# Kernel tuning notes

Hardware: AMD Instinct MI355X
Metric: run time of the kernel (lower is better)

Reference implementation:

```python
import jax, jax.numpy as jnp
import numpy as np

N_NODES = 100000
N_EDGES = 1600000
N_GRAPHS = 256
EPS = 1e-5  # GraphNorm / BatchNorm eps


def _seg_sum(x, seg, n):
    return jax.ops.segment_sum(x, seg, num_segments=n)


def setup_inputs() -> dict:
    key = jax.random.key(0)
    ks = jax.random.split(key, 24)
    f32 = jnp.float32

    def nrm(k, shape, s=0.05):
        return jax.random.normal(k, shape, f32) * s

    inp = {}
    inp["x"] = jax.random.normal(ks[0], (N_NODES, 64), f32)
    inp["edge_attr"] = jax.random.normal(ks[1], (N_EDGES, 8), f32)
    # edge_mlp: Linear(8,16) -> ReLU -> Linear(16,1); final bias +2 keeps degrees positive
    inp["em_w1"] = nrm(ks[2], (16, 8), 0.1); inp["em_b1"] = jnp.zeros((16,), f32)
    inp["em_w2"] = nrm(ks[3], (1, 16), 0.1); inp["em_b2"] = jnp.full((1,), 2.0, f32)
    # GCNConv weights stored (in, out); PyG GCNConv lin has no bias, separate bias after aggregation
    inp["conv_w0"] = nrm(ks[4], (64, 128)); inp["conv_b0"] = jnp.zeros((128,), f32)
    inp["conv_w1"] = nrm(ks[5], (128, 128)); inp["conv_b1"] = jnp.zeros((128,), f32)
    inp["conv_w2"] = nrm(ks[6], (128, 128)); inp["conv_b2"] = jnp.zeros((128,), f32)
    # GraphNorm params: weight=1, bias=0, mean_scale=1 (PyG init)
    for i in range(3):
        inp[f"gn_w{i}"] = jnp.ones((128,), f32)
        inp[f"gn_b{i}"] = jnp.zeros((128,), f32)
        inp[f"gn_ms{i}"] = jnp.ones((128,), f32)
    # MLP head (weights stored (in,out)); BatchNorm1d eval: running_mean=0, running_var=1
    inp["lin_w0"] = nrm(ks[7], (128, 256)); inp["lin_b0"] = jnp.zeros((256,), f32)
    inp["bn_g0"] = jnp.ones((256,), f32); inp["bn_b0"] = jnp.zeros((256,), f32)
    inp["lin_w1"] = nrm(ks[8], (256, 128)); inp["lin_b1"] = jnp.zeros((128,), f32)
    inp["bn_g1"] = jnp.ones((128,), f32); inp["bn_b1"] = jnp.zeros((128,), f32)
    inp["out_w"] = nrm(ks[9], (128, 1)); inp["out_b"] = jnp.zeros((1,), f32)
    inp["edge_index"] = jax.random.randint(ks[10], (2, N_EDGES), 0, N_NODES)
    inp["batch"] = jnp.sort(jax.random.randint(ks[11], (N_NODES,), 0, N_GRAPHS))
    return inp


def _gcn_conv(h, W, b, src, tgt, ew):
    # PyG GCNConv with edge_weight: add self-loops (weight 1), symmetric normalization
    hw = h @ W  # [N, out]
    deg = _seg_sum(ew, tgt, N_NODES) + 1.0  # in-degree incl. self-loop
    dinv = jnp.where(deg > 0, jax.lax.rsqrt(deg), 0.0)
    norm_e = dinv[src] * ew * dinv[tgt]  # [E]
    agg = _seg_sum(norm_e[:, None] * hw[src], tgt, N_NODES)
    agg = agg + (dinv * dinv)[:, None] * hw  # self-loop contribution
    return agg + b


def _graph_norm(h, batch, w, b, ms, cnt):
    mean = _seg_sum(h, batch, N_GRAPHS) / cnt[:, None]  # [G, C]
    sub = h - ms * mean[batch]
    var = _seg_sum(sub * sub, batch, N_GRAPHS) / cnt[:, None]
    return w * sub / jnp.sqrt(var + EPS)[batch] + b


def reference(x, edge_attr, em_w1, em_b1, em_w2, em_b2,
              conv_w0, conv_b0, conv_w1, conv_b1, conv_w2, conv_b2,
              gn_w0, gn_b0, gn_ms0, gn_w1, gn_b1, gn_ms1, gn_w2, gn_b2, gn_ms2,
              lin_w0, lin_b0, bn_g0, bn_b0, lin_w1, lin_b1, bn_g1, bn_b1,
              out_w, out_b, edge_index, batch):
    src, tgt = edge_index[0], edge_index[1]
    ew = (jax.nn.relu(edge_attr @ em_w1.T + em_b1) @ em_w2.T + em_b2).reshape(-1)  # [E]
    cnt = jnp.maximum(_seg_sum(jnp.ones((N_NODES,), x.dtype), batch, N_GRAPHS), 1.0)

    h = x
    layers = [(conv_w0, conv_b0, gn_w0, gn_b0, gn_ms0),
              (conv_w1, conv_b1, gn_w1, gn_b1, gn_ms1),
              (conv_w2, conv_b2, gn_w2, gn_b2, gn_ms2)]
    for W, b, gw, gb, gms in layers:
        h = _gcn_conv(h, W, b, src, tgt, ew)
        h = _graph_norm(h, batch, gw, gb, gms, cnt)
        h = jax.nn.relu(h)  # dropout is identity in eval mode

    pooled = _seg_sum(h, batch, N_GRAPHS) / cnt[:, None]  # global_mean_pool [G, 128]

    inv = 1.0 / jnp.sqrt(1.0 + EPS)  # BatchNorm1d eval: mean=0, var=1
    h = jax.nn.relu((pooled @ lin_w0 + lin_b0) * inv * bn_g0 + bn_b0)
    h = jax.nn.relu((h @ lin_w1 + lin_b1) * inv * bn_g1 + bn_b1)
    out = h @ out_w + out_b  # [G, 1]
    return (out, h)
```

## Files before the change

kernel.cpp:

```cpp
#include <hip/hip_runtime.h>

#define N_NODES 100000
#define N_EDGES 1600000
#define N_GRAPHS 256
#define EPS 1e-5f

#define SCAN_BLOCKS ((N_NODES + 255) / 256)

#define EB 6250
#define WB 128
#define W0B 32
#define PREP_BLOCKS (EB + WB + W0B + 2)

typedef __attribute__((ext_vector_type(8))) short bfrag8;
typedef __attribute__((ext_vector_type(4))) float facc4;

__device__ __forceinline__ void fma4(float4& a, float s, const float4& w) {
  a.x += s * w.x; a.y += s * w.y; a.z += s * w.z; a.w += s * w.w;
}

__device__ __forceinline__ unsigned short f2bf(float f) {
  union { float f; unsigned u; } x;
  x.f = f;
  unsigned r = x.u + 0x7FFF + ((x.u >> 16) & 1);
  return (unsigned short)(r >> 16);
}
__device__ __forceinline__ unsigned packbf(float a, float b) {
  return (unsigned)f2bf(a) | ((unsigned)f2bf(b) << 16);
}
__device__ __forceinline__ float4 bf4(unsigned lo, unsigned hi) {
  union { unsigned u; float f; } a, b, c, d;
  a.u = lo << 16;
  b.u = lo & 0xFFFF0000u;
  c.u = hi << 16;
  d.u = hi & 0xFFFF0000u;
  return make_float4(a.f, b.f, c.f, d.f);
}
__device__ __forceinline__ float bfat(const unsigned* tb, int idx) {
  unsigned u = tb[idx >> 1];
  union { unsigned u; float f; } v;
  v.u = (idx & 1) ? (u & 0xFFFF0000u) : (u << 16);
  return v.f;
}

__global__ __launch_bounds__(256) void k_prep(
    const float* __restrict__ ea, const float* __restrict__ w1,
    const float* __restrict__ b1, const float* __restrict__ w2,
    const float* __restrict__ b2, const int* __restrict__ tgt,
    float* __restrict__ ew, int* __restrict__ rowcnt, int* __restrict__ rank,
    const float* __restrict__ cw1, const float* __restrict__ cw2,
    unsigned short* __restrict__ wt1, unsigned short* __restrict__ wt2,
    const float* __restrict__ cw0, unsigned short* __restrict__ wt0,
    const int* __restrict__ batch, int* __restrict__ start) {
  __shared__ float W1[128], B1[16], W2[16];
  const int b = blockIdx.x;
  const int t = threadIdx.x;
  if (b < EB) {
    if (t < 128) W1[t] = w1[t];
    if (t < 16) { B1[t] = b1[t]; W2[t] = w2[t]; }
    __syncthreads();
    int e = b * 256 + t;
    if (e >= N_EDGES) return;
    const float4* ap = (const float4*)(ea + (size_t)e * 8);
    float4 a0 = ap[0], a1 = ap[1];
    float a[8] = {a0.x, a0.y, a0.z, a0.w, a1.x, a1.y, a1.z, a1.w};
    float out = b2[0];
#pragma unroll
    for (int i = 0; i < 16; ++i) {
      float h = B1[i];
#pragma unroll
      for (int j = 0; j < 8; ++j) h += a[j] * W1[i * 8 + j];
      out += fmaxf(h, 0.f) * W2[i];
    }
    ew[e] = out;
    rank[e] = atomicAdd(&rowcnt[tgt[e]], 1);
  } else if (b < EB + WB) {
    int lb = b - EB;
    int half = lb >> 6;
    int id = (lb & 63) * 256 + t;
    const float* w = half ? cw2 : cw1;
    unsigned short* o = half ? wt2 : wt1;
    int n = id >> 7, k = id & 127;
    o[n * 128 + k] = f2bf(w[k * 128 + n]);
  } else if (b < EB + WB + W0B) {
    int id = (b - EB - WB) * 256 + t;
    if (id >= 8192) return;
    int n = id >> 6, k = id & 63;
    wt0[n * 64 + k] = f2bf(cw0[k * 128 + n]);
  } else {
    int g = (b - EB - WB - W0B) * 256 + t;
    if (g > N_GRAPHS) return;
    int lo = 0, hi = N_NODES;
    while (lo < hi) {
      int mid = (lo + hi) >> 1;
      if (batch[mid] < g) lo = mid + 1; else hi = mid;
    }
    start[g] = lo;
  }
}

__global__ __launch_bounds__(256) void k_scan1(const int* __restrict__ cnt,
                                               int* __restrict__ bsum) {
  int i = blockIdx.x * 256 + threadIdx.x;
  int v = (i < N_NODES) ? cnt[i] : 0;
#pragma unroll
  for (int off = 32; off; off >>= 1) v += __shfl_down(v, off);
  __shared__ int ws[4];
  if ((threadIdx.x & 63) == 0) ws[threadIdx.x >> 6] = v;
  __syncthreads();
  if (threadIdx.x == 0) bsum[blockIdx.x] = ws[0] + ws[1] + ws[2] + ws[3];
}

__global__ __launch_bounds__(512) void k_scan2(const int* __restrict__ bsum,
                                               int* __restrict__ boff) {
  __shared__ int s[512];
  int t = threadIdx.x;
  s[t] = (t < SCAN_BLOCKS) ? bsum[t] : 0;
  __syncthreads();
  for (int off = 1; off < 512; off <<= 1) {
    int u = (t >= off) ? s[t - off] : 0;
    __syncthreads();
    s[t] += u;
    __syncthreads();
  }
  boff[t] = (t == 0) ? 0 : s[t - 1];
}

__global__ __launch_bounds__(256) void k_scan3(const int* __restrict__ cnt,
                                               const int* __restrict__ boff,
                                               int* __restrict__ rowstart) {
  __shared__ int s[256];
  int t = threadIdx.x;
  int i = blockIdx.x * 256 + t;
  int v = (i < N_NODES) ? cnt[i] : 0;
  s[t] = v;
  __syncthreads();
  for (int off = 1; off < 256; off <<= 1) {
    int u = (t >= off) ? s[t - off] : 0;
    __syncthreads();
    s[t] += u;
    __syncthreads();
  }
  if (i < N_NODES) {
    int pre = boff[blockIdx.x] + s[t] - v;
    rowstart[i] = pre;
    if (i == N_NODES - 1) rowstart[N_NODES] = pre + v;
  }
}

__global__ __launch_bounds__(256) void k_fill(
    const int* __restrict__ src, const int* __restrict__ tgt,
    const float* __restrict__ ew, const int* __restrict__ rank,
    const int* __restrict__ rowstart, uint2* __restrict__ meta) {
  int e = blockIdx.x * 256 + threadIdx.x;
  if (e >= N_EDGES) return;
  int p = rowstart[tgt[e]] + rank[e];
  union { float f; unsigned u; } w;
  w.f = ew[e];
  meta[p] = make_uint2(w.u, (unsigned)src[e]);
}

__global__ __launch_bounds__(256) void k_degcvt(
    const uint2* __restrict__ meta, const int* __restrict__ rowstart,
    const float* __restrict__ x, float* __restrict__ dinv,
    unsigned* __restrict__ xb) {
  const int n = blockIdx.x * 4 + (threadIdx.x >> 6);
  if (n >= N_NODES) return;
  const int lane = threadIdx.x & 63;
  const int rs = rowstart[n], re = rowstart[n + 1];
  float s = 0.f;
  for (int j = rs + lane; j < re; j += 64) {
    union { unsigned u; float f; } w;
    w.u = meta[j].x;
    s += w.f;
  }
#pragma unroll
  for (int m = 1; m < 64; m <<= 1) s += __shfl_xor(s, m);
  float d = 1.f + s;
  float dv = d > 0.f ? rsqrtf(d) : 0.f;
  if (lane == 0) dinv[n] = dv;
  if (lane < 32) {
    float2 v = ((const float2*)x)[(size_t)n * 32 + lane];
    xb[((unsigned)n << 5) + lane] = packbf(dv * v.x, dv * v.y);
  }
}

__global__ __launch_bounds__(256) void k_gather64b(
    const unsigned* __restrict__ xb, const uint2* __restrict__ meta,
    const int* __restrict__ rowstart, const float* __restrict__ dinv,
    unsigned* __restrict__ aggxb) {
  const int t = threadIdx.x;
  const int n = blockIdx.x * 4 + (t >> 6);
  if (n >= N_NODES) return;
  const unsigned lane = t & 63;
  const unsigned q = lane >> 3;
  const unsigned cl = lane & 7;
  const int rs = rowstart[n], re = rowstart[n + 1];
  const uint4* x4 = (const uint4*)xb;
  float4 lo0 = make_float4(0.f, 0.f, 0.f, 0.f), hi0 = lo0;
  float4 lo1 = lo0, hi1 = lo0;
  int j = rs;
  for (; j + 16 <= re; j += 16) {
    uint2 m0 = meta[j + q], m1 = meta[j + 8 + q];
    union { unsigned u; float f; } w0, w1;
    w0.u = m0.x; w1.u = m1.x;
    uint4 v0 = x4[(m0.y << 3) + cl];
    uint4 v1 = x4[(m1.y << 3) + cl];
    fma4(lo0, w0.f, bf4(v0.x, v0.y));
    fma4(hi0, w0.f, bf4(v0.z, v0.w));
    fma4(lo1, w1.f, bf4(v1.x, v1.y));
    fma4(hi1, w1.f, bf4(v1.z, v1.w));
  }
  for (; j + 8 <= re; j += 8) {
    uint2 m0 = meta[j + q];
    union { unsigned u; float f; } w0;
    w0.u = m0.x;
    uint4 v0 = x4[(m0.y << 3) + cl];
    fma4(lo0, w0.f, bf4(v0.x, v0.y));
    fma4(hi0, w0.f, bf4(v0.z, v0.w));
  }
  if (j + (int)q < re) {
    uint2 m0 = meta[j + q];
    union { unsigned u; float f; } w0;
    w0.u = m0.x;
    uint4 v0 = x4[(m0.y << 3) + cl];
    fma4(lo1, w0.f, bf4(v0.x, v0.y));
    fma4(hi1, w0.f, bf4(v0.z, v0.w));
  }
  lo0.x += lo1.x; lo0.y += lo1.y; lo0.z += lo1.z; lo0.w += lo1.w;
  hi0.x += hi1.x; hi0.y += hi1.y; hi0.z += hi1.z; hi0.w += hi1.w;
#pragma unroll
  for (int m = 8; m <= 32; m <<= 1) {
    lo0.x += __shfl_xor(lo0.x, m);
    lo0.y += __shfl_xor(lo0.y, m);
    lo0.z += __shfl_xor(lo0.z, m);
    lo0.w += __shfl_xor(lo0.w, m);
    hi0.x += __shfl_xor(hi0.x, m);
    hi0.y += __shfl_xor(hi0.y, m);
    hi0.z += __shfl_xor(hi0.z, m);
    hi0.w += __shfl_xor(hi0.w, m);
  }
  if (q == 0) {
    float dv = dinv[n];
    uint4 sv = x4[((unsigned)n << 3) + cl];
    float4 slo = bf4(sv.x, sv.y), shi = bf4(sv.z, sv.w);
    uint4 o;
    o.x = packbf(dv * (lo0.x + slo.x), dv * (lo0.y + slo.y));
    o.y = packbf(dv * (lo0.z + slo.z), dv * (lo0.w + slo.w));
    o.z = packbf(dv * (hi0.x + shi.x), dv * (hi0.y + shi.y));
    o.w = packbf(dv * (hi0.z + shi.z), dv * (hi0.w + shi.w));
    ((uint4*)aggxb)[((unsigned)n << 3) + cl] = o;
  }
}

__global__ __launch_bounds__(256) void k_hw_mfma0(
    const unsigned short* __restrict__ aggxb,
    const unsigned short* __restrict__ wt0, const float* __restrict__ bias,
    unsigned short* __restrict__ h1b) {
  __shared__ unsigned short Asb[64][72];
  __shared__ unsigned short Wsb[128][72];
  const int t = threadIdx.x;
  const int base = blockIdx.x * 64;

  for (int i = t; i < 1024; i += 256) {
    int nr = i >> 3, k8 = (i & 7) * 8;
    *(uint4*)&Wsb[nr][k8] = *(const uint4*)&wt0[nr * 64 + k8];
  }
  {
    const int ln = t >> 2;
    const int kp = (t & 3) * 16;
    const int n = base + ln;
    if (n < N_NODES) {
      *(uint4*)&Asb[ln][kp] = *(const uint4*)&aggxb[(size_t)n * 64 + kp];
      *(uint4*)&Asb[ln][kp + 8] = *(const uint4*)&aggxb[(size_t)n * 64 + kp + 8];
    } else {
      uint4 z = make_uint4(0, 0, 0, 0);
      *(uint4*)&Asb[ln][kp] = z;
      *(uint4*)&Asb[ln][kp + 8] = z;
    }
  }
  __syncthreads();

  const int wv = t >> 6;
  const int lr = t & 15;
  const int lk = (t >> 4) & 3;
  const int m0 = wv * 16;

  bfrag8 af[2];
#pragma unroll
  for (int kc = 0; kc < 2; ++kc)
    af[kc] = *(const bfrag8*)&Asb[m0 + lr][kc * 32 + lk * 8];

#pragma unroll
  for (int nt = 0; nt < 8; ++nt) {
    facc4 c = {0.f, 0.f, 0.f, 0.f};
#pragma unroll
    for (int kc = 0; kc < 2; ++kc) {
      bfrag8 bf = *(const bfrag8*)&Wsb[nt * 16 + lr][kc * 32 + lk * 8];
      c = __builtin_amdgcn_mfma_f32_16x16x32_bf16(af[kc], bf, c, 0, 0, 0);
    }
    int col = nt * 16 + lr;
    float bv = bias[col];
#pragma unroll
    for (int r = 0; r < 4; ++r) {
      int n = base + m0 + lk * 4 + r;
      if (n < N_NODES) h1b[(size_t)n * 128 + col] = f2bf(c[r] + bv);
    }
  }
}

__global__ __launch_bounds__(256) void k_hw_mfma(
    const unsigned* __restrict__ hb, const unsigned short* __restrict__ wt,
    const int* __restrict__ batch, const float* __restrict__ An,
    const float* __restrict__ Bn, const float* __restrict__ dinv,
    unsigned short* __restrict__ hwb) {
  __shared__ unsigned short Asb[64][136];
  __shared__ unsigned short Wsb[128][136];
  const int t = threadIdx.x;
  const int base = blockIdx.x * 64;

  for (int i = t; i < 2048; i += 256) {
    int nr = i >> 4, k8 = (i & 15) * 8;
    *(uint4*)&Wsb[nr][k8] = *(const uint4*)&wt[nr * 128 + k8];
  }
  {
    const int ln = t >> 2;
    const int cg = (t & 3) * 32;
    const int n = base + ln;
    if (n < N_NODES) {
      const int g = batch[n];
      const uint4* hp = (const uint4*)(hb + (size_t)n * 64);
      const float* Ap = An + (size_t)g * 128;
      const float* Bp = Bn + (size_t)g * 128;
#pragma unroll
      for (int qq = 0; qq < 4; ++qq) {
        int c = cg + qq * 8;
        uint4 v = hp[(t & 3) * 4 + qq];
        float4 lo = bf4(v.x, v.y);
        float4 hi = bf4(v.z, v.w);
        float4 Alo = *(const float4*)&Ap[c], Blo = *(const float4*)&Bp[c];
        float4 Ahi = *(const float4*)&Ap[c + 4], Bhi = *(const float4*)&Bp[c + 4];
        uint4 o;
        o.x = packbf(fmaxf(Alo.x * lo.x + Blo.x, 0.f),
                     fmaxf(Alo.y * lo.y + Blo.y, 0.f));
        o.y = packbf(fmaxf(Alo.z * lo.z + Blo.z, 0.f),
                     fmaxf(Alo.w * lo.w + Blo.w, 0.f));
        o.z = packbf(fmaxf(Ahi.x * hi.x + Bhi.x, 0.f),
                     fmaxf(Ahi.y * hi.y + Bhi.y, 0.f));
        o.w = packbf(fmaxf(Ahi.z * hi.z + Bhi.z, 0.f),
                     fmaxf(Ahi.w * hi.w + Bhi.w, 0.f));
        *(uint4*)&Asb[ln][c] = o;
      }
    } else {
      uint4 z = make_uint4(0, 0, 0, 0);
#pragma unroll
      for (int qq = 0; qq < 4; ++qq) *(uint4*)&Asb[ln][cg + qq * 8] = z;
    }
  }
  __syncthreads();

  const int wv = t >> 6;
  const int lr = t & 15;
  const int lk = (t >> 4) & 3;
  const int m0 = wv * 16;

  bfrag8 af[4];
#pragma unroll
  for (int kc = 0; kc < 4; ++kc)
    af[kc] = *(const bfrag8*)&Asb[m0 + lr][kc * 32 + lk * 8];

  float dv[4];
#pragma unroll
  for (int r = 0; r < 4; ++r) {
    int n = base + m0 + lk * 4 + r;
    dv[r] = (n < N_NODES) ? dinv[n] : 0.f;
  }

#pragma unroll
  for (int nt = 0; nt < 8; ++nt) {
    facc4 c = {0.f, 0.f, 0.f, 0.f};
#pragma unroll
    for (int kc = 0; kc < 4; ++kc) {
      bfrag8 bf = *(const bfrag8*)&Wsb[nt * 16 + lr][kc * 32 + lk * 8];
      c = __builtin_amdgcn_mfma_f32_16x16x32_bf16(af[kc], bf, c, 0, 0, 0);
    }
    int col = nt * 16 + lr;
#pragma unroll
    for (int r = 0; r < 4; ++r) {
      int n = base + m0 + lk * 4 + r;
      if (n < N_NODES) hwb[(size_t)n * 128 + col] = f2bf(dv[r] * c[r]);
    }
  }
}

__global__ __launch_bounds__(256) void k_gatherb(
    const unsigned* __restrict__ hwb, const uint2* __restrict__ meta,
    const int* __restrict__ rowstart, const float* __restrict__ dinv,
    const float* __restrict__ bias, unsigned* __restrict__ aggb) {
  const int t = threadIdx.x;
  const int n = blockIdx.x * 4 + (t >> 6);
  if (n >= N_NODES) return;
  const unsigned lane = t & 63;
  const unsigned q = lane >> 4;
  const unsigned cl = lane & 15;
  const int rs = rowstart[n], re = rowstart[n + 1];
  const uint4* hb4 = (const uint4*)hwb;
  float4 lo0 = make_float4(0.f, 0.f, 0.f, 0.f), hi0 = lo0;
  float4 lo1 = lo0, hi1 = lo0;
  int j = rs;
  for (; j + 8 <= re; j += 8) {
    uint2 m0 = meta[j + q], m1 = meta[j + 4 + q];
    union { unsigned u; float f; } w0, w1;
    w0.u = m0.x; w1.u = m1.x;
    uint4 v0 = hb4[(m0.y << 4) + cl];
    uint4 v1 = hb4[(m1.y << 4) + cl];
    fma4(lo0, w0.f, bf4(v0.x, v0.y));
    fma4(hi0, w0.f, bf4(v0.z, v0.w));
    fma4(lo1, w1.f, bf4(v1.x, v1.y));
    fma4(hi1, w1.f, bf4(v1.z, v1.w));
  }
  for (; j + 4 <= re; j += 4) {
    uint2 m0 = meta[j + q];
    union { unsigned u; float f; } w0;
    w0.u = m0.x;
    uint4 v0 = hb4[(m0.y << 4) + cl];
    fma4(lo0, w0.f, bf4(v0.x, v0.y));
    fma4(hi0, w0.f, bf4(v0.z, v0.w));
  }
  if (j + (int)q < re) {
    uint2 m0 = meta[j + q];
    union { unsigned u; float f; } w0;
    w0.u = m0.x;
    uint4 v0 = hb4[(m0.y << 4) + cl];
    fma4(lo1, w0.f, bf4(v0.x, v0.y));
    fma4(hi1, w0.f, bf4(v0.z, v0.w));
  }
  lo0.x += lo1.x; lo0.y += lo1.y; lo0.z += lo1.z; lo0.w += lo1.w;
  hi0.x += hi1.x; hi0.y += hi1.y; hi0.z += hi1.z; hi0.w += hi1.w;
#pragma unroll
  for (int m = 16; m <= 32; m <<= 1) {
    lo0.x += __shfl_xor(lo0.x, m);
    lo0.y += __shfl_xor(lo0.y, m);
    lo0.z += __shfl_xor(lo0.z, m);
    lo0.w += __shfl_xor(lo0.w, m);
    hi0.x += __shfl_xor(hi0.x, m);
    hi0.y += __shfl_xor(hi0.y, m);
    hi0.z += __shfl_xor(hi0.z, m);
    hi0.w += __shfl_xor(hi0.w, m);
  }
  if (q == 0) {
    float dv = dinv[n];
    uint4 sv = hb4[((unsigned)n << 4) + cl];
    float4 slo = bf4(sv.x, sv.y), shi = bf4(sv.z, sv.w);
    float4 blo = *(const float4*)&bias[cl * 8];
    float4 bhi = *(const float4*)&bias[cl * 8 + 4];
    uint4 o;
    o.x = packbf(dv * (lo0.x + slo.x) + blo.x, dv * (lo0.y + slo.y) + blo.y);
    o.y = packbf(dv * (lo0.z + slo.z) + blo.z, dv * (lo0.w + slo.w) + blo.w);
    o.z = packbf(dv * (hi0.x + shi.x) + bhi.x, dv * (hi0.y + shi.y) + bhi.y);
    o.w = packbf(dv * (hi0.z + shi.z) + bhi.z, dv * (hi0.w + shi.w) + bhi.w);
    ((uint4*)aggb)[((unsigned)n << 4) + cl] = o;
  }
}

__global__ __launch_bounds__(512) void k_gstats(
    const unsigned* __restrict__ hb, const int* __restrict__ start,
    const float* __restrict__ gw, const float* __restrict__ gb,
    const float* __restrict__ gms, float* __restrict__ An,
    float* __restrict__ Bn) {
  int g = blockIdx.x;
  int s = start[g], e = start[g + 1];
  int t = threadIdx.x, p = t >> 7, c = t & 127;
  float sum = 0.f, sq = 0.f;
  for (int n = s + p; n < e; n += 4) {
    float v = bfat(hb + (size_t)n * 64, c);
    sum += v;
    sq += v * v;
  }
  __shared__ float S[4][128], Q[4][128];
  S[p][c] = sum;
  Q[p][c] = sq;
  __syncthreads();
  if (t < 128) {
    float cnt = (float)max(e - s, 1);
    float mean = (S[0][t] + S[1][t] + S[2][t] + S[3][t]) / cnt;
    float e2 = (Q[0][t] + Q[1][t] + Q[2][t] + Q[3][t]) / cnt;
    float ms = gms[t];
    float var = fmaxf(e2 - ms * (2.f - ms) * mean * mean, 0.f);
    float scale = gw[t] / sqrtf(var + EPS);
    An[(size_t)g * 128 + t] = scale;
    Bn[(size_t)g * 128 + t] = gb[t] - scale * ms * mean;
  }
}

__global__ __launch_bounds__(512) void k_pool(
    const unsigned* __restrict__ hb, const int* __restrict__ start,
    const float* __restrict__ An, const float* __restrict__ Bn,
    float* __restrict__ pooled) {
  int g = blockIdx.x;
  int s = start[g], e = start[g + 1];
  int t = threadIdx.x, p = t >> 7, c = t & 127;
  float A = An[(size_t)g * 128 + c], B = Bn[(size_t)g * 128 + c];
  float sum = 0.f;
  for (int n = s + p; n < e; n += 4)
    sum += fmaxf(A * bfat(hb + (size_t)n * 64, c) + B, 0.f);
  __shared__ float S[4][128];
  S[p][c] = sum;
  __syncthreads();
  if (t < 128) {
    float cnt = (float)max(e - s, 1);
    pooled[g * 128 + t] = (S[0][t] + S[1][t] + S[2][t] + S[3][t]) / cnt;
  }
}

__global__ __launch_bounds__(256) void k_head(
    const float* __restrict__ pooled, const float* __restrict__ w0,
    const float* __restrict__ b0, const float* __restrict__ g0,
    const float* __restrict__ bb0, const float* __restrict__ w1,
    const float* __restrict__ b1, const float* __restrict__ g1,
    const float* __restrict__ bb1, const float* __restrict__ ow,
    const float* __restrict__ ob, float* __restrict__ out) {
  __shared__ float p[128], h1[256], h2[128];
  int g = blockIdx.x, t = threadIdx.x;
  const float inv = 1.0f / sqrtf(1.0f + EPS);
  if (t < 128) p[t] = pooled[g * 128 + t];
  __syncthreads();
  {
    float acc = b0[t];
#pragma unroll 8
    for (int k = 0; k < 128; ++k) acc += p[k] * w0[k * 256 + t];
    h1[t] = fmaxf(acc * inv * g0[t] + bb0[t], 0.f);
  }
  __syncthreads();
  if (t < 128) {
    float acc = b1[t];
#pragma unroll 8
    for (int k = 0; k < 256; ++k) acc += h1[k] * w1[k * 128 + t];
    float v = fmaxf(acc * inv * g1[t] + bb1[t], 0.f);
    h2[t] = v;
    out[N_GRAPHS + g * 128 + t] = v;
  }
  __syncthreads();
  if (t < 64) {
    float v = h2[t] * ow[t] + h2[t + 64] * ow[t + 64];
#pragma unroll
    for (int off = 32; off; off >>= 1) v += __shfl_down(v, off);
    if (t == 0) out[g] = v + ob[0];
  }
}

extern "C" void kernel_launch(void* const* d_in, const int* in_sizes, int n_in,
                              void* d_out, int out_size, void* d_ws,
                              size_t ws_size, hipStream_t stream) {
  const float* x = (const float*)d_in[0];
  const float* edge_attr = (const float*)d_in[1];
  const float* em_w1 = (const float*)d_in[2];
  const float* em_b1 = (const float*)d_in[3];
  const float* em_w2 = (const float*)d_in[4];
  const float* em_b2 = (const float*)d_in[5];
  const float* conv_w[3] = {(const float*)d_in[6], (const float*)d_in[8],
                            (const float*)d_in[10]};
  const float* conv_b[3] = {(const float*)d_in[7], (const float*)d_in[9],
                            (const float*)d_in[11]};
  const float* gn_w[3] = {(const float*)d_in[12], (const float*)d_in[15],
                          (const float*)d_in[18]};
  const float* gn_b[3] = {(const float*)d_in[13], (const float*)d_in[16],
                          (const float*)d_in[19]};
  const float* gn_ms[3] = {(const float*)d_in[14], (const float*)d_in[17],
                           (const float*)d_in[20]};
  const float* lin_w0 = (const float*)d_in[21];
  const float* lin_b0 = (const float*)d_in[22];
  const float* bn_g0 = (const float*)d_in[23];
  const float* bn_b0 = (const float*)d_in[24];
  const float* lin_w1 = (const float*)d_in[25];
  const float* lin_b1 = (const float*)d_in[26];
  const float* bn_g1 = (const float*)d_in[27];
  const float* bn_b1 = (const float*)d_in[28];
  const float* out_w = (const float*)d_in[29];
  const float* out_b = (const float*)d_in[30];
  const int* edge_index = (const int*)d_in[31];
  const int* batch = (const int*)d_in[32];
  const int* src = edge_index;
  const int* tgt = edge_index + N_EDGES;

  char* w = (char*)d_ws;
  size_t off = 0;
  auto carve = [&](size_t bytes) {
    void* p = w + off;
    off = (off + bytes + 511) & ~(size_t)511;
    return p;
  };
  float* ew = (float*)carve((size_t)N_EDGES * 4);
  int* rank = (int*)carve((size_t)N_EDGES * 4);
  float* dinv = (float*)carve((size_t)N_NODES * 4);
  int* rowcnt = (int*)carve((size_t)N_NODES * 4);
  int* rowstart = (int*)carve((size_t)(N_NODES + 1) * 4);
  int* bsum = (int*)carve((size_t)SCAN_BLOCKS * 4);
  int* boff = (int*)carve((size_t)512 * 4);
  uint2* meta = (uint2*)carve((size_t)N_EDGES * 8);
  int* start = (int*)carve((N_GRAPHS + 1) * 4);
  float* AB = (float*)carve((size_t)6 * N_GRAPHS * 128 * 4);
  unsigned* xb = (unsigned*)carve((size_t)N_NODES * 64 * 2);
  unsigned* aggxb = (unsigned*)carve((size_t)N_NODES * 64 * 2);
  unsigned* h1b = (unsigned*)carve((size_t)N_NODES * 128 * 2);
  unsigned* hwb = (unsigned*)carve((size_t)N_NODES * 128 * 2);
  unsigned* agg1b = (unsigned*)carve((size_t)N_NODES * 128 * 2);
  unsigned* agg2b = (unsigned*)carve((size_t)N_NODES * 128 * 2);
  unsigned short* wt0 = (unsigned short*)carve((size_t)128 * 64 * 2);
  unsigned short* wt1 = (unsigned short*)carve((size_t)128 * 128 * 2);
  unsigned short* wt2 = (unsigned short*)carve((size_t)128 * 128 * 2);
  float* pooled = (float*)carve((size_t)N_GRAPHS * 128 * 4);

  float* A0 = AB, *B0 = AB + N_GRAPHS * 128;
  float* A1 = AB + 2 * N_GRAPHS * 128, *B1 = AB + 3 * N_GRAPHS * 128;
  float* A2 = AB + 4 * N_GRAPHS * 128, *B2 = AB + 5 * N_GRAPHS * 128;

  hipMemsetAsync(rowcnt, 0, (size_t)N_NODES * 4, stream);

  k_prep<<<PREP_BLOCKS, 256, 0, stream>>>(
      edge_attr, em_w1, em_b1, em_w2, em_b2, tgt, ew, rowcnt, rank,
      conv_w[1], conv_w[2], wt1, wt2, conv_w[0], wt0, batch, start);
  k_scan1<<<SCAN_BLOCKS, 256, 0, stream>>>(rowcnt, bsum);
  k_scan2<<<1, 512, 0, stream>>>(bsum, boff);
  k_scan3<<<SCAN_BLOCKS, 256, 0, stream>>>(rowcnt, boff, rowstart);
  k_fill<<<(N_EDGES + 255) / 256, 256, 0, stream>>>(src, tgt, ew, rank,
                                                    rowstart, meta);

  const int ggrid = (N_NODES + 3) / 4;
  const int hwgrid = (N_NODES + 63) / 64;

  k_degcvt<<<ggrid, 256, 0, stream>>>(meta, rowstart, x, dinv, xb);

  k_gather64b<<<ggrid, 256, 0, stream>>>(xb, meta, rowstart, dinv, aggxb);
  k_hw_mfma0<<<hwgrid, 256, 0, stream>>>((unsigned short*)aggxb, wt0,
                                         conv_b[0], (unsigned short*)h1b);
  k_gstats<<<N_GRAPHS, 512, 0, stream>>>(h1b, start, gn_w[0], gn_b[0],
                                         gn_ms[0], A0, B0);
  k_hw_mfma<<<hwgrid, 256, 0, stream>>>(h1b, wt1, batch, A0, B0, dinv,
                                        (unsigned short*)hwb);
  k_gatherb<<<ggrid, 256, 0, stream>>>(hwb, meta, rowstart, dinv, conv_b[1],
                                       agg1b);
  k_gstats<<<N_GRAPHS, 512, 0, stream>>>(agg1b, start, gn_w[1], gn_b[1],
                                         gn_ms[1], A1, B1);
  k_hw_mfma<<<hwgrid, 256, 0, stream>>>(agg1b, wt2, batch, A1, B1, dinv,
                                        (unsigned short*)hwb);
  k_gatherb<<<ggrid, 256, 0, stream>>>(hwb, meta, rowstart, dinv, conv_b[2],
                                       agg2b);
  k_gstats<<<N_GRAPHS, 512, 0, stream>>>(agg2b, start, gn_w[2], gn_b[2],
                                         gn_ms[2], A2, B2);

  k_pool<<<N_GRAPHS, 512, 0, stream>>>(agg2b, start, A2, B2, pooled);
  k_head<<<N_GRAPHS, 256, 0, stream>>>(pooled, lin_w0, lin_b0, bn_g0, bn_b0,
                                       lin_w1, lin_b1, bn_g1, bn_b1, out_w,
                                       out_b, (float*)d_out);
}
```

Baseline: 525.5 us.

## Build CSR via two-level bucket sort instead of global atomic counting

```diff
diff --git a/kernel.cpp b/kernel.cpp
--- a/kernel.cpp
+++ b/kernel.cpp
@@ -5,7 +5,10 @@
 #define N_GRAPHS 256
 #define EPS 1e-5f
 
-#define SCAN_BLOCKS ((N_NODES + 255) / 256)
+#define NBUCK 1024
+#define NUSED 782
+#define NBLK 128
+#define EPB (N_EDGES / NBLK)
 
 #define EB 6250
 #define WB 128
@@ -46,8 +49,7 @@
 __global__ __launch_bounds__(256) void k_prep(
     const float* __restrict__ ea, const float* __restrict__ w1,
     const float* __restrict__ b1, const float* __restrict__ w2,
-    const float* __restrict__ b2, const int* __restrict__ tgt,
-    float* __restrict__ ew, int* __restrict__ rowcnt, int* __restrict__ rank,
+    const float* __restrict__ b2, float* __restrict__ ew,
     const float* __restrict__ cw1, const float* __restrict__ cw2,
     unsigned short* __restrict__ wt1, unsigned short* __restrict__ wt2,
     const float* __restrict__ cw0, unsigned short* __restrict__ wt0,
@@ -73,7 +75,6 @@
       out += fmaxf(h, 0.f) * W2[i];
     }
     ew[e] = out;
-    rank[e] = atomicAdd(&rowcnt[tgt[e]], 1);
   } else if (b < EB + WB) {
     int lb = b - EB;
     int half = lb >> 6;
@@ -99,65 +100,96 @@
   }
 }
 
-__global__ __launch_bounds__(256) void k_scan1(const int* __restrict__ cnt,
-                                               int* __restrict__ bsum) {
-  int i = blockIdx.x * 256 + threadIdx.x;
-  int v = (i < N_NODES) ? cnt[i] : 0;
-#pragma unroll
-  for (int off = 32; off; off >>= 1) v += __shfl_down(v, off);
-  __shared__ int ws[4];
-  if ((threadIdx.x & 63) == 0) ws[threadIdx.x >> 6] = v;
-  __syncthreads();
-  if (threadIdx.x == 0) bsum[blockIdx.x] = ws[0] + ws[1] + ws[2] + ws[3];
-}
-
-__global__ __launch_bounds__(512) void k_scan2(const int* __restrict__ bsum,
-                                               int* __restrict__ boff) {
-  __shared__ int s[512];
-  int t = threadIdx.x;
-  s[t] = (t < SCAN_BLOCKS) ? bsum[t] : 0;
-  __syncthreads();
-  for (int off = 1; off < 512; off <<= 1) {
-    int u = (t >= off) ? s[t - off] : 0;
+__global__ __launch_bounds__(256) void k_hist(const int* __restrict__ tgt,
+                                              int* __restrict__ hists) {
+  __shared__ int h[NBUCK];
+  const int blk = blockIdx.x, t = threadIdx.x;
+  for (int i = t; i < NBUCK; i += 256) h[i] = 0;
+  __syncthreads();
+  const int s = blk * EPB, e = s + EPB;
+  for (int j = s + t; j < e; j += 256) atomicAdd(&h[tgt[j] >> 7], 1);
+  __syncthreads();
+  for (int i = t; i < NBUCK; i += 256) hists[blk * NBUCK + i] = h[i];
+}
+
+__global__ __launch_bounds__(1024) void k_bscan(const int* __restrict__ hists,
+                                                int* __restrict__ bbase,
+                                                int* __restrict__ cursor) {
+  __shared__ int s[NBUCK];
+  const int b = threadIdx.x;
+  int tot = 0;
+  for (int k = 0; k < NBLK; ++k) tot += hists[k * NBUCK + b];
+  s[b] = tot;
+  __syncthreads();
+  for (int off = 1; off < NBUCK; off <<= 1) {
+    int u = (b >= off) ? s[b - off] : 0;
     __syncthreads();
-    s[t] += u;
+    s[b] += u;
     __syncthreads();
   }
-  boff[t] = (t == 0) ? 0 : s[t - 1];
-}
-
-__global__ __launch_bounds__(256) void k_scan3(const int* __restrict__ cnt,
-                                               const int* __restrict__ boff,
-                                               int* __restrict__ rowstart) {
-  __shared__ int s[256];
-  int t = threadIdx.x;
-  int i = blockIdx.x * 256 + t;
-  int v = (i < N_NODES) ? cnt[i] : 0;
-  s[t] = v;
-  __syncthreads();
-  for (int off = 1; off < 256; off <<= 1) {
-    int u = (t >= off) ? s[t - off] : 0;
+  int base = s[b] - tot;
+  bbase[b] = base;
+  if (b == NBUCK - 1) bbase[NBUCK] = N_EDGES;
+  int c = base;
+  for (int k = 0; k < NBLK; ++k) {
+    cursor[k * NBUCK + b] = c;
+    c += hists[k * NBUCK + b];
+  }
+}
+
+__global__ __launch_bounds__(256) void k_scatter(
+    const int* __restrict__ src, const int* __restrict__ tgt,
+    const float* __restrict__ ew, const int* __restrict__ cursor,
+    uint2* __restrict__ mb) {
+  __shared__ int cur[NBUCK];
+  const int blk = blockIdx.x, t = threadIdx.x;
+  for (int i = t; i < NBUCK; i += 256) cur[i] = cursor[blk * NBUCK + i];
+  __syncthreads();
+  const int s = blk * EPB, e = s + EPB;
+  for (int j = s + t; j < e; j += 256) {
+    int d = tgt[j];
+    int bin = d >> 7;
+    int pos = atomicAdd(&cur[bin], 1);
+    union { float f; unsigned u; } w;
+    w.f = ew[j];
+    mb[pos] = make_uint2(w.u, (unsigned)src[j] | ((unsigned)(d & 127) << 25));
+  }
+}
+
+__global__ __launch_bounds__(256) void k_csr(const uint2* __restrict__ mb,
+                                             const int* __restrict__ bbase,
+                                             uint2* __restrict__ meta,
+                                             int* __restrict__ rowstart) {
+  __shared__ int hist[128];
+  __shared__ int cur[128];
+  const int b = blockIdx.x;
+  const int t = threadIdx.x;
+  const int s = bbase[b], e = bbase[b + 1];
+  if (t < 128) hist[t] = 0;
+  __syncthreads();
+  for (int j = s + t; j < e; j += 256)
+    atomicAdd(&hist[mb[j].y >> 25], 1);
+  __syncthreads();
+  int own = (t < 128) ? hist[t] : 0;
+  for (int off = 1; off < 128; off <<= 1) {
+    int u = (t >= off && t < 128) ? hist[t - off] : 0;
     __syncthreads();
-    s[t] += u;
+    if (t < 128) hist[t] += u;
     __syncthreads();
   }
-  if (i < N_NODES) {
-    int pre = boff[blockIdx.x] + s[t] - v;
-    rowstart[i] = pre;
-    if (i == N_NODES - 1) rowstart[N_NODES] = pre + v;
-  }
-}
-
-__global__ __launch_bounds__(256) void k_fill(
-    const int* __restrict__ src, const int* __restrict__ tgt,
-    const float* __restrict__ ew, const int* __restrict__ rank,
-    const int* __restrict__ rowstart, uint2* __restrict__ meta) {
-  int e = blockIdx.x * 256 + threadIdx.x;
-  if (e >= N_EDGES) return;
-  int p = rowstart[tgt[e]] + rank[e];
-  union { float f; unsigned u; } w;
-  w.f = ew[e];
-  meta[p] = make_uint2(w.u, (unsigned)src[e]);
+  if (t < 128) {
+    int excl = hist[t] - own;
+    int node = b * 128 + t;
+    if (node <= N_NODES) rowstart[node] = s + excl;
+    cur[t] = s + excl;
+  }
+  __syncthreads();
+  for (int j = s + t; j < e; j += 256) {
+    uint2 m = mb[j];
+    int bin = m.y >> 25;
+    int pos = atomicAdd(&cur[bin], 1);
+    meta[pos] = make_uint2(m.x, m.y & 0x1FFFFFFu);
+  }
 }
 
 __global__ __launch_bounds__(256) void k_degcvt(
@@ -591,12 +623,12 @@
     return p;
   };
   float* ew = (float*)carve((size_t)N_EDGES * 4);
-  int* rank = (int*)carve((size_t)N_EDGES * 4);
   float* dinv = (float*)carve((size_t)N_NODES * 4);
-  int* rowcnt = (int*)carve((size_t)N_NODES * 4);
   int* rowstart = (int*)carve((size_t)(N_NODES + 1) * 4);
-  int* bsum = (int*)carve((size_t)SCAN_BLOCKS * 4);
-  int* boff = (int*)carve((size_t)512 * 4);
+  int* hists = (int*)carve((size_t)NBLK * NBUCK * 4);
+  int* cursor = (int*)carve((size_t)NBLK * NBUCK * 4);
+  int* bbase = (int*)carve((size_t)(NBUCK + 1) * 4);
+  uint2* mb = (uint2*)carve((size_t)N_EDGES * 8);
   uint2* meta = (uint2*)carve((size_t)N_EDGES * 8);
   int* start = (int*)carve((N_GRAPHS + 1) * 4);
   float* AB = (float*)carve((size_t)6 * N_GRAPHS * 128 * 4);
@@ -615,16 +647,13 @@
   float* A1 = AB + 2 * N_GRAPHS * 128, *B1 = AB + 3 * N_GRAPHS * 128;
   float* A2 = AB + 4 * N_GRAPHS * 128, *B2 = AB + 5 * N_GRAPHS * 128;
 
-  hipMemsetAsync(rowcnt, 0, (size_t)N_NODES * 4, stream);
-
   k_prep<<<PREP_BLOCKS, 256, 0, stream>>>(
-      edge_attr, em_w1, em_b1, em_w2, em_b2, tgt, ew, rowcnt, rank,
-      conv_w[1], conv_w[2], wt1, wt2, conv_w[0], wt0, batch, start);
-  k_scan1<<<SCAN_BLOCKS, 256, 0, stream>>>(rowcnt, bsum);
-  k_scan2<<<1, 512, 0, stream>>>(bsum, boff);
-  k_scan3<<<SCAN_BLOCKS, 256, 0, stream>>>(rowcnt, boff, rowstart);
-  k_fill<<<(N_EDGES + 255) / 256, 256, 0, stream>>>(src, tgt, ew, rank,
-                                                    rowstart, meta);
+      edge_attr, em_w1, em_b1, em_w2, em_b2, ew, conv_w[1], conv_w[2], wt1,
+      wt2, conv_w[0], wt0, batch, start);
+  k_hist<<<NBLK, 256, 0, stream>>>(tgt, hists);
+  k_bscan<<<1, 1024, 0, stream>>>(hists, bbase, cursor);
+  k_scatter<<<NBLK, 256, 0, stream>>>(src, tgt, ew, cursor, mb);
+  k_csr<<<NUSED, 256, 0, stream>>>(mb, bbase, meta, rowstart);
 
   const int ggrid = (N_NODES + 3) / 4;
   const int hwgrid = (N_NODES + 63) / 64;
```

Measured after the change: 523.2 us. About the same (-0.4%).
